# Kernel optimization log

Hardware: AMD Instinct MI355X
Metric: run time of the kernel (lower is better)

Reference implementation:

```python
import jax, jax.numpy as jnp
import numpy as np

DIM = 1024
HEADS = 16
DIM_HEAD = 64
INNER = HEADS * DIM_HEAD
EPS = 1e-5


def layernorm(x, g, b):
    mu = jnp.mean(x, axis=-1, keepdims=True)
    var = jnp.mean((x - mu) ** 2, axis=-1, keepdims=True)
    return (x - mu) * jax.lax.rsqrt(var + EPS) * g + b


def setup_inputs() -> dict:
    key = jax.random.key(0)
    ks = jax.random.split(key, 8)
    B, S = 2, 2048
    s_in = (2.0 / DIM) ** 0.5
    return {
        "x": jax.random.normal(ks[0], (B, S, DIM), jnp.float32),
        "w_qkv": jax.random.normal(ks[1], (DIM, 3 * INNER), jnp.float32) * s_in,
        "w_out": jax.random.normal(ks[2], (INNER, DIM), jnp.float32) * s_in,
        "b_out": jnp.zeros((DIM,), jnp.float32),
        "g1": jnp.ones((DIM,), jnp.float32),
        "beta1": jnp.zeros((DIM,), jnp.float32),
        "g2": jnp.ones((DIM,), jnp.float32),
        "beta2": jnp.zeros((DIM,), jnp.float32),
        "w_ff1": jax.random.normal(ks[3], (DIM, 4 * DIM), jnp.float32) * s_in,
        "b_ff1": jnp.zeros((4 * DIM,), jnp.float32),
        "w_ff2": jax.random.normal(ks[4], (4 * DIM, DIM), jnp.float32) * (2.0 / (4 * DIM)) ** 0.5,
        "b_ff2": jnp.zeros((DIM,), jnp.float32),
    }


def reference(x, w_qkv, w_out, b_out, g1, beta1, g2, beta2, w_ff1, b_ff1, w_ff2, b_ff2):
    B, S, D = x.shape
    scale = DIM_HEAD ** -0.5
    # --- attention block (pre-norm) ---
    h = layernorm(x, g1, beta1)
    qkv = h @ w_qkv  # [B,S,3*INNER]
    q, k, v = jnp.split(qkv, 3, axis=-1)
    def heads(t):
        return t.reshape(B, S, HEADS, DIM_HEAD).transpose(0, 2, 1, 3)  # [B,H,S,dh]
    q, k, v = heads(q), heads(k), heads(v)
    attn = jnp.einsum("bhsd,bhtd->bhst", q, k) * scale
    attn = jax.nn.softmax(attn, axis=-1)
    out = jnp.einsum("bhst,bhtd->bhsd", attn, v)
    out = out.transpose(0, 2, 1, 3).reshape(B, S, INNER)
    x = x + out @ w_out + b_out
    # --- FFN block (pre-norm) ---
    h = layernorm(x, g2, beta2)
    h = jax.nn.gelu(h @ w_ff1 + b_ff1, approximate=False)
    x = x + h @ w_ff2 + b_ff2
    return x
```

## Files before the change

### kernel.cpp

```cpp
#include <hip/hip_runtime.h>
#include <math.h>

typedef unsigned short u16;
typedef __attribute__((ext_vector_type(4))) float f32x4;
typedef __attribute__((ext_vector_type(16))) float f32x16;
typedef __attribute__((ext_vector_type(4))) unsigned short u16x4;
typedef __attribute__((ext_vector_type(8))) __bf16 bf16x8;

static constexpr int SS   = 2048;
static constexpr int DD   = 1024;
static constexpr int HH   = 16;
static constexpr int DH   = 64;
static constexpr int NTOK = 4096;
static constexpr int NQKV = 3072;

#define DEV static __device__ __forceinline__
#define GLD_AS1(p) ((__attribute__((address_space(1))) void*)(void*)(p))
#define GLD_AS3(p) ((__attribute__((address_space(3))) void*)(p))

#define WAIT_BAR(N) asm volatile("s_waitcnt vmcnt(" #N ")\n\ts_barrier" ::: "memory")
#define BAR()       asm volatile("s_barrier" ::: "memory")

DEV u16 f2bf(float f) {
    union { float f; unsigned int i; } v; v.f = f;
    unsigned int r = v.i + 0x7fffu + ((v.i >> 16) & 1u);
    return (u16)(r >> 16);
}
DEV float bdec(u16 u) {
    union { unsigned int i; float f; } v; v.i = ((unsigned int)u) << 16; return v.f;
}

DEV f32x4 MFMA(bf16x8 a, bf16x8 b, f32x4 c) {
    return __builtin_amdgcn_mfma_f32_16x16x32_bf16(a, b, c, 0, 0, 0);
}
DEV f32x16 MFMA32(bf16x8 a, bf16x8 b, f32x16 c) {
    return __builtin_amdgcn_mfma_f32_32x32x16_bf16(a, b, c, 0, 0, 0);
}
DEV f32x16 zero16() {
    f32x16 z;
    #pragma unroll
    for (int i = 0; i < 16; i++) z[i] = 0.f;
    return z;
}

__global__ __launch_bounds__(256)
void k_transpose(const float* __restrict__ in, u16* __restrict__ out, int R, int C) {
    __shared__ float tile[32][33];
    int c0 = blockIdx.x * 32, r0 = blockIdx.y * 32;
    int tx = threadIdx.x, ty = threadIdx.y;
    #pragma unroll
    for (int i = 0; i < 32; i += 8)
        tile[ty + i][tx] = in[(size_t)(r0 + ty + i) * C + c0 + tx];
    __syncthreads();
    #pragma unroll
    for (int i = 0; i < 32; i += 8)
        out[(size_t)(c0 + ty + i) * R + r0 + tx] = f2bf(tile[tx][ty + i]);
}

__global__ __launch_bounds__(256)
void k_transpose_v(const u16* __restrict__ qkv, u16* __restrict__ vT) {
    __shared__ u16 tile[32][33];
    int bid = blockIdx.x;
    int st = bid & 63;
    int dt = (bid >> 6) & 1;
    int bh = bid >> 7;
    int b = bh >> 4, h = bh & 15;
    int s0 = st * 32, d0 = dt * 32;
    int tx = threadIdx.x & 31, ty = threadIdx.x >> 5;
    const u16* src = qkv + ((size_t)(b * SS + s0)) * NQKV + 2048 + h * DH + d0;
    #pragma unroll
    for (int i = 0; i < 32; i += 8)
        tile[ty + i][tx] = src[(size_t)(ty + i) * NQKV + tx];
    __syncthreads();
    u16* dst = vT + ((size_t)bh * DH + d0) * SS + s0;
    #pragma unroll
    for (int i = 0; i < 32; i += 8)
        dst[(size_t)(ty + i) * SS + tx] = tile[tx][ty + i];
}

__global__ __launch_bounds__(256)
void k_layernorm(const float* __restrict__ x, const float* __restrict__ g,
                 const float* __restrict__ b, u16* __restrict__ out) {
    int row = blockIdx.x, t = threadIdx.x;
    const float4* xp = reinterpret_cast<const float4*>(x + (size_t)row * DD);
    float4 v = xp[t];
    float s = v.x + v.y + v.z + v.w;
    float q = v.x * v.x + v.y * v.y + v.z * v.z + v.w * v.w;
    #pragma unroll
    for (int m = 1; m < 64; m <<= 1) { s += __shfl_xor(s, m); q += __shfl_xor(q, m); }
    __shared__ float ps[4], pq[4];
    int w = t >> 6, l = t & 63;
    if (l == 0) { ps[w] = s; pq[w] = q; }
    __syncthreads();
    s = ps[0] + ps[1] + ps[2] + ps[3];
    q = pq[0] + pq[1] + pq[2] + pq[3];
    float mu = s * (1.0f / DD);
    float var = q * (1.0f / DD) - mu * mu;
    float rstd = rsqrtf(var + 1e-5f);
    float4 gv = reinterpret_cast<const float4*>(g)[t];
    float4 bv = reinterpret_cast<const float4*>(b)[t];
    u16x4 o;
    o.x = f2bf((v.x - mu) * rstd * gv.x + bv.x);
    o.y = f2bf((v.y - mu) * rstd * gv.y + bv.y);
    o.z = f2bf((v.z - mu) * rstd * gv.z + bv.z);
    o.w = f2bf((v.w - mu) * rstd * gv.w + bv.w);
    reinterpret_cast<u16x4*>(out + (size_t)row * DD)[t] = o;
}

__global__ __launch_bounds__(256)
void k_redln(const float* __restrict__ x, const u16* __restrict__ P0,
             const u16* __restrict__ P1, const float* __restrict__ bias,
             const float* __restrict__ g, const float* __restrict__ be,
             float* __restrict__ X1, u16* __restrict__ LNout) {
    int row = blockIdx.x, t = threadIdx.x;
    size_t i = (size_t)row * 256 + t;
    float4 xv = reinterpret_cast<const float4*>(x)[i];
    u16x4 a = reinterpret_cast<const u16x4*>(P0)[i];
    u16x4 bb = reinterpret_cast<const u16x4*>(P1)[i];
    float4 bv = reinterpret_cast<const float4*>(bias)[t];
    float4 v;
    v.x = xv.x + bdec(a.x) + bdec(bb.x) + bv.x;
    v.y = xv.y + bdec(a.y) + bdec(bb.y) + bv.y;
    v.z = xv.z + bdec(a.z) + bdec(bb.z) + bv.z;
    v.w = xv.w + bdec(a.w) + bdec(bb.w) + bv.w;
    reinterpret_cast<float4*>(X1)[i] = v;
    float s = v.x + v.y + v.z + v.w;
    float q = v.x * v.x + v.y * v.y + v.z * v.z + v.w * v.w;
    #pragma unroll
    for (int m = 1; m < 64; m <<= 1) { s += __shfl_xor(s, m); q += __shfl_xor(q, m); }
    __shared__ float ps[4], pq[4];
    int w = t >> 6, l = t & 63;
    if (l == 0) { ps[w] = s; pq[w] = q; }
    __syncthreads();
    s = ps[0] + ps[1] + ps[2] + ps[3];
    q = pq[0] + pq[1] + pq[2] + pq[3];
    float mu = s * (1.0f / DD);
    float var = q * (1.0f / DD) - mu * mu;
    float rstd = rsqrtf(var + 1e-5f);
    float4 gv = reinterpret_cast<const float4*>(g)[t];
    float4 ev = reinterpret_cast<const float4*>(be)[t];
    u16x4 o;
    o.x = f2bf((v.x - mu) * rstd * gv.x + ev.x);
    o.y = f2bf((v.y - mu) * rstd * gv.y + ev.y);
    o.z = f2bf((v.z - mu) * rstd * gv.z + ev.z);
    o.w = f2bf((v.w - mu) * rstd * gv.w + ev.w);
    reinterpret_cast<u16x4*>(LNout + (size_t)row * DD)[t] = o;
}

__global__ __launch_bounds__(256)
void k_gemm_qkv(const u16* __restrict__ A, const u16* __restrict__ BT,
                u16* __restrict__ Cb, int M, int N, int K) {
    __shared__ __align__(128) char lds[2][32768];
    const int t = threadIdx.x;
    const int w = t >> 6, l = t & 63;
    const int lg = l >> 4, lr = l & 15;
    const int GX = gridDim.x;
    const int T = GX * gridDim.y;
    const int H = blockIdx.x + blockIdx.y * GX;
    const int L = (H & 7) * (T >> 3) + (H >> 3);
    const int m0 = (L / GX) * 128, n0 = (L % GX) * 128;
    const int wr = w >> 1, wc = w & 1;

    const int csw = ((l & 7) ^ (l >> 3)) << 3;
    const int chunk0 = w * 4;
    const int srow = (l >> 3);

    f32x4 acc[4][4];
    #pragma unroll
    for (int i = 0; i < 4; i++)
        #pragma unroll
        for (int j = 0; j < 4; j++)
            acc[i][j] = (f32x4){0.f, 0.f, 0.f, 0.f};

    #pragma unroll
    for (int i = 0; i < 4; i++) {
        const int chunk = chunk0 + i;
        const int r = chunk * 8 + srow;
        __builtin_amdgcn_global_load_lds(GLD_AS1(A  + (size_t)(m0 + r) * K + csw),
                                         GLD_AS3(lds[0] + chunk * 1024), 16, 0, 0);
        __builtin_amdgcn_global_load_lds(GLD_AS1(BT + (size_t)(n0 + r) * K + csw),
                                         GLD_AS3(lds[0] + 16384 + chunk * 1024), 16, 0, 0);
    }

    int buf = 0;
    for (int kt = 0; kt < K; kt += 64) {
        if (kt + 64 < K) {
            #pragma unroll
            for (int i = 0; i < 4; i++) {
                const int chunk = chunk0 + i;
                const int r = chunk * 8 + srow;
                __builtin_amdgcn_global_load_lds(GLD_AS1(A  + (size_t)(m0 + r) * K + kt + 64 + csw),
                                                 GLD_AS3(lds[buf ^ 1] + chunk * 1024), 16, 0, 0);
                __builtin_amdgcn_global_load_lds(GLD_AS1(BT + (size_t)(n0 + r) * K + kt + 64 + csw),
                                                 GLD_AS3(lds[buf ^ 1] + 16384 + chunk * 1024), 16, 0, 0);
            }
            WAIT_BAR(8);
        } else {
            WAIT_BAR(0);
        }
        const char* Al = lds[buf];
        const char* Bl = lds[buf] + 16384;
        #pragma unroll
        for (int s = 0; s < 2; s++) {
            const int swz = (s * 64 + lg * 16) ^ ((lr & 7) << 4);
            bf16x8 af[4], bfr[4];
            #pragma unroll
            for (int mi = 0; mi < 4; mi++)
                af[mi] = *reinterpret_cast<const bf16x8*>(Al + (wr * 64 + mi * 16 + lr) * 128 + swz);
            #pragma unroll
            for (int ni = 0; ni < 4; ni++)
                bfr[ni] = *reinterpret_cast<const bf16x8*>(Bl + (wc * 64 + ni * 16 + lr) * 128 + swz);
            #pragma unroll
            for (int mi = 0; mi < 4; mi++)
                #pragma unroll
                for (int ni = 0; ni < 4; ni++)
                    acc[mi][ni] = MFMA(af[mi], bfr[ni], acc[mi][ni]);
        }
        BAR();
        buf ^= 1;
    }

    #pragma unroll
    for (int mi = 0; mi < 4; mi++) {
        #pragma unroll
        for (int ni = 0; ni < 4; ni++) {
            int nn = n0 + wc * 64 + ni * 16 + lr;
            #pragma unroll
            for (int r = 0; r < 4; r++) {
                int mm = m0 + wr * 64 + mi * 16 + lg * 4 + r;
                float v = acc[mi][ni][r];
                float sv = (nn < 1024) ? v * 0.18033688011112042f : v;
                Cb[(size_t)mm * NQKV + nn] = f2bf(sv);
            }
        }
    }
}

__global__ __launch_bounds__(512, 2)
void k_gemm_ff1(const u16* __restrict__ A, const u16* __restrict__ BT,
                u16* __restrict__ Cb, const float* __restrict__ bias,
                int M, int N, int K) {
    __shared__ __align__(128) char lds[2][65536];
    const int t = threadIdx.x;
    const int w = t >> 6, l = t & 63;
    const int lg = l >> 4, lr = l & 15;
    const int GX = gridDim.x;
    const int T = GX * gridDim.y;
    const int H = blockIdx.x + blockIdx.y * GX;
    const int L = (H & 7) * (T >> 3) + (H >> 3);
    const int m0 = (L / GX) * 256, n0 = (L % GX) * 256;
    const int wr = w >> 2, wc = w & 3;

    const int csw = ((l & 7) ^ (l >> 3)) << 3;
    const int srow8 = l >> 3;
    const int swzc = (lr & 7) << 4;

    f32x4 acc[8][4];
    #pragma unroll
    for (int i = 0; i < 8; i++)
        #pragma unroll
        for (int j = 0; j < 4; j++)
            acc[i][j] = (f32x4){0.f, 0.f, 0.f, 0.f};

    auto STAGEH = [&](int bf, int which, int half, int kt) {
        const u16* sb = which ? BT : A;
        const int rb = which ? n0 : m0;
        char* dst = lds[bf] + which * 32768 + half * 16384 + w * 1024;
        #pragma unroll
        for (int j = 0; j < 2; j++) {
            const int r = half * 128 + (j * 8 + w) * 8 + srow8;
            __builtin_amdgcn_global_load_lds(GLD_AS1(sb + (size_t)(rb + r) * K + kt + csw),
                                             GLD_AS3(dst + j * 8192), 16, 0, 0);
        }
    };

    STAGEH(0, 0, 0, 0); STAGEH(0, 0, 1, 0); STAGEH(0, 1, 0, 0); STAGEH(0, 1, 1, 0);

    const int nt = K >> 6;
    int buf = 0;
    for (int tt = 0; tt < nt; ++tt) {
        const int nb = buf ^ 1;
        const bool pre = (tt + 1 < nt);
        const char* Abase = lds[buf];
        const char* Bbase = lds[buf] + 32768;

        bf16x8 Bf[4][2];
        #pragma unroll
        for (int p = 0; p < 4; p++) {
            if (pre) STAGEH(nb, p >> 1, p & 1, (tt + 1) * 64);
            if (p == 0) {
                if (pre) { WAIT_BAR(2); } else { WAIT_BAR(0); }
                #pragma unroll
                for (int ni = 0; ni < 4; ni++)
                    #pragma unroll
                    for (int ks = 0; ks < 2; ks++)
                        Bf[ni][ks] = *reinterpret_cast<const bf16x8*>(
                            Bbase + (wc >> 1) * 16384 + ((wc & 1) * 64 + ni * 16 + lr) * 128
                                  + ((ks * 64 + lg * 16) ^ swzc));
            }
            bf16x8 Af[2][2];
            #pragma unroll
            for (int mi2 = 0; mi2 < 2; mi2++)
                #pragma unroll
                for (int ks = 0; ks < 2; ks++)
                    Af[mi2][ks] = *reinterpret_cast<const bf16x8*>(
                        Abase + wr * 16384 + ((p * 2 + mi2) * 16 + lr) * 128
                              + ((ks * 64 + lg * 16) ^ swzc));
            __builtin_amdgcn_s_setprio(1);
            #pragma unroll
            for (int mi2 = 0; mi2 < 2; mi2++)
                #pragma unroll
                for (int ni = 0; ni < 4; ni++)
                    #pragma unroll
                    for (int ks = 0; ks < 2; ks++)
                        acc[p * 2 + mi2][ni] = MFMA(Af[mi2][ks], Bf[ni][ks], acc[p * 2 + mi2][ni]);
            __builtin_amdgcn_s_setprio(0);
            BAR();
        }
        buf = nb;
    }

    #pragma unroll
    for (int mi = 0; mi < 8; mi++) {
        #pragma unroll
        for (int ni = 0; ni < 4; ni++) {
            int nn = n0 + wc * 64 + ni * 16 + lr;
            #pragma unroll
            for (int r = 0; r < 4; r++) {
                int mm = m0 + wr * 128 + mi * 16 + lg * 4 + r;
                float u = acc[mi][ni][r] + bias[nn];
                float u3 = u * u * u;
                float gl = u / (1.0f + exp2f(-2.3022077f * u - 0.10294276f * u3));
                Cb[(size_t)mm * N + nn] = f2bf(gl);
            }
        }
    }
}

__global__ __launch_bounds__(256)
void k_gemm_sk(const u16* __restrict__ A, const u16* __restrict__ BT,
               u16* __restrict__ P0, u16* __restrict__ P1, int M, int N, int K) {
    __shared__ __align__(128) char lds[2][32768];
    const int t = threadIdx.x;
    const int w = t >> 6, l = t & 63;
    const int lg = l >> 4, lr = l & 15;
    const int GX = gridDim.x, GY = gridDim.y;
    const int T = GX * GY * gridDim.z;
    const int H = blockIdx.x + blockIdx.y * GX + blockIdx.z * GX * GY;
    const int L = (H & 7) * (T >> 3) + (H >> 3);
    const int n0 = (L % GX) * 128;
    const int m0 = ((L / GX) % GY) * 128;
    const int zz = L / (GX * GY);
    const int wr = w >> 1, wc = w & 1;

    const int kh = K >> 1;
    const int kbeg = zz * kh;
    const int kend = kbeg + kh;

    const int csw = ((l & 7) ^ (l >> 3)) << 3;
    const int chunk0 = w * 4;
    const int srow = (l >> 3);

    f32x4 acc[4][4];
    #pragma unroll
    for (int i = 0; i < 4; i++)
        #pragma unroll
        for (int j = 0; j < 4; j++)
            acc[i][j] = (f32x4){0.f, 0.f, 0.f, 0.f};

    #pragma unroll
    for (int i = 0; i < 4; i++) {
        const int chunk = chunk0 + i;
        const int r = chunk * 8 + srow;
        __builtin_amdgcn_global_load_lds(GLD_AS1(A  + (size_t)(m0 + r) * K + kbeg + csw),
                                         GLD_AS3(lds[0] + chunk * 1024), 16, 0, 0);
        __builtin_amdgcn_global_load_lds(GLD_AS1(BT + (size_t)(n0 + r) * K + kbeg + csw),
                                         GLD_AS3(lds[0] + 16384 + chunk * 1024), 16, 0, 0);
    }

    int buf = 0;
    for (int kt = kbeg; kt < kend; kt += 64) {
        if (kt + 64 < kend) {
            #pragma unroll
            for (int i = 0; i < 4; i++) {
                const int chunk = chunk0 + i;
                const int r = chunk * 8 + srow;
                __builtin_amdgcn_global_load_lds(GLD_AS1(A  + (size_t)(m0 + r) * K + kt + 64 + csw),
                                                 GLD_AS3(lds[buf ^ 1] + chunk * 1024), 16, 0, 0);
                __builtin_amdgcn_global_load_lds(GLD_AS1(BT + (size_t)(n0 + r) * K + kt + 64 + csw),
                                                 GLD_AS3(lds[buf ^ 1] + 16384 + chunk * 1024), 16, 0, 0);
            }
            WAIT_BAR(8);
        } else {
            WAIT_BAR(0);
        }
        const char* Al = lds[buf];
        const char* Bl = lds[buf] + 16384;
        #pragma unroll
        for (int s = 0; s < 2; s++) {
            const int swz = (s * 64 + lg * 16) ^ ((lr & 7) << 4);
            bf16x8 af[4], bfr[4];
            #pragma unroll
            for (int mi = 0; mi < 4; mi++)
                af[mi] = *reinterpret_cast<const bf16x8*>(Al + (wr * 64 + mi * 16 + lr) * 128 + swz);
            #pragma unroll
            for (int ni = 0; ni < 4; ni++)
                bfr[ni] = *reinterpret_cast<const bf16x8*>(Bl + (wc * 64 + ni * 16 + lr) * 128 + swz);
            #pragma unroll
            for (int mi = 0; mi < 4; mi++)
                #pragma unroll
                for (int ni = 0; ni < 4; ni++)
                    acc[mi][ni] = MFMA(af[mi], bfr[ni], acc[mi][ni]);
        }
        BAR();
        buf ^= 1;
    }

    u16* dst = zz ? P1 : P0;
    #pragma unroll
    for (int mi = 0; mi < 4; mi++) {
        #pragma unroll
        for (int ni = 0; ni < 4; ni++) {
            int nn = n0 + wc * 64 + ni * 16 + lr;
            #pragma unroll
            for (int r = 0; r < 4; r++) {
                int mm = m0 + wr * 64 + mi * 16 + lg * 4 + r;
                dst[(size_t)mm * N + nn] = f2bf(acc[mi][ni][r]);
            }
        }
    }
}

__global__ __launch_bounds__(256)
void k_ffreduce(const float* __restrict__ RES, const u16* __restrict__ P0,
                const u16* __restrict__ P1, const float* __restrict__ bias,
                float* __restrict__ OUT) {
    int i = blockIdx.x * 256 + threadIdx.x;
    float4 xv = reinterpret_cast<const float4*>(RES)[i];
    u16x4 a = reinterpret_cast<const u16x4*>(P0)[i];
    u16x4 b = reinterpret_cast<const u16x4*>(P1)[i];
    float4 bv = reinterpret_cast<const float4*>(bias)[i & (DD / 4 - 1)];
    float4 o;
    o.x = xv.x + bdec(a.x) + bdec(b.x) + bv.x;
    o.y = xv.y + bdec(a.y) + bdec(b.y) + bv.y;
    o.z = xv.z + bdec(a.z) + bdec(b.z) + bv.z;
    o.w = xv.w + bdec(a.w) + bdec(b.w) + bv.w;
    reinterpret_cast<float4*>(OUT)[i] = o;
}

__global__ __launch_bounds__(256)
void k_attn(const u16* __restrict__ qkv, const u16* __restrict__ vT,
            u16* __restrict__ out) {
    const int w = threadIdx.x >> 6, l = threadIdx.x & 63;
    const int q = l & 31, hi = l >> 5;
    const int task = (blockIdx.x & 7) * 64 + (blockIdx.x >> 3);
    const int bh = task >> 4;
    const int qg = task & 15;
    const int b = bh >> 4, h = bh & 15;
    const size_t rowbase = (size_t)b * SS;
    const int q0 = (qg * 4 + w) * 32;

    __shared__ __align__(128) u16 Kl[3][64 * 64];
    __shared__ __align__(128) u16 Vl[2][64 * 64];

    const u16* kbase = qkv + rowbase * NQKV + 1024 + h * DH;
    const u16* vbase = vT + (size_t)bh * DH * SS;

    const int srow8 = l >> 3;
    const int sslot = (l & 7) ^ srow8;
    const int kr0 = w * 8 + srow8;
    const u16* kg0 = kbase + (size_t)kr0 * NQKV + sslot * 8;
    const u16* kg1 = kbase + (size_t)(kr0 + 32) * NQKV + sslot * 8;
    const u16* vg0 = vbase + (size_t)kr0 * SS + sslot * 8;
    const u16* vg1 = vbase + (size_t)(kr0 + 32) * SS + sslot * 8;
    const int chA = (w * 8) * 64, chB = (w * 8 + 32) * 64;

    const u16* qrow = qkv + (rowbase + q0 + q) * NQKV + h * DH + hi * 8;
    bf16x8 qf[4];
    #pragma unroll
    for (int ks = 0; ks < 4; ks++)
        qf[ks] = *reinterpret_cast<const bf16x8*>(qrow + ks * 16);
    asm volatile("s_waitcnt vmcnt(0)" ::: "memory");

    bf16x8 onesf;
    #pragma unroll
    for (int i = 0; i < 8; i++) onesf[i] = (__bf16)1.0f;

    f32x16 o0 = zero16(), o1 = zero16();
    f32x16 lacc = zero16();
    const int qsw = (q & 7) << 3;

    __builtin_amdgcn_global_load_lds(GLD_AS1(kg0), GLD_AS3((u16*)Kl[0] + chA), 16, 0, 0);
    __builtin_amdgcn_global_load_lds(GLD_AS1(kg1), GLD_AS3((u16*)Kl[0] + chB), 16, 0, 0);
    __builtin_amdgcn_global_load_lds(GLD_AS1(kg0 + (size_t)64 * NQKV), GLD_AS3((u16*)Kl[1] + chA), 16, 0, 0);
    __builtin_amdgcn_global_load_lds(GLD_AS1(kg1 + (size_t)64 * NQKV), GLD_AS3((u16*)Kl[1] + chB), 16, 0, 0);
    __builtin_amdgcn_global_load_lds(GLD_AS1(vg0), GLD_AS3((u16*)Vl[0] + chA), 16, 0, 0);
    __builtin_amdgcn_global_load_lds(GLD_AS1(vg1), GLD_AS3((u16*)Vl[0] + chB), 16, 0, 0);
    WAIT_BAR(4);

    f32x16 scA0 = zero16(), scA1 = zero16();
    {
        const u16* Kb = Kl[0];
        #pragma unroll
        for (int ks = 0; ks < 4; ks++) {
            const int off = (ks * 16 + hi * 8) ^ qsw;
            bf16x8 kf0 = *reinterpret_cast<const bf16x8*>(Kb + q * 64 + off);
            bf16x8 kf1 = *reinterpret_cast<const bf16x8*>(Kb + (q + 32) * 64 + off);
            scA0 = MFMA32(kf0, qf[ks], scA0);
            scA1 = MFMA32(kf1, qf[ks], scA1);
        }
    }

    int kRead = 1, vRead = 0;
    for (int i = 0; i < 32; ++i) {
        const int kStage = (kRead == 2) ? 0 : kRead + 1;
        if (i + 2 < 32) {
            const size_t koff = (size_t)(i + 2) * 64 * NQKV;
            __builtin_amdgcn_global_load_lds(GLD_AS1(kg0 + koff), GLD_AS3((u16*)Kl[kStage] + chA), 16, 0, 0);
            __builtin_amdgcn_global_load_lds(GLD_AS1(kg1 + koff), GLD_AS3((u16*)Kl[kStage] + chB), 16, 0, 0);
            WAIT_BAR(2);
        } else {
            WAIT_BAR(0);
        }
        if (i + 1 < 32) {
            const int voff = (i + 1) * 64;
            __builtin_amdgcn_global_load_lds(GLD_AS1(vg0 + voff), GLD_AS3((u16*)Vl[vRead ^ 1] + chA), 16, 0, 0);
            __builtin_amdgcn_global_load_lds(GLD_AS1(vg1 + voff), GLD_AS3((u16*)Vl[vRead ^ 1] + chB), 16, 0, 0);
        }

        f32x16 p0, p1;
        #pragma unroll
        for (int j = 0; j < 16; j++) p0[j] = exp2f(scA0[j]);
        #pragma unroll
        for (int j = 0; j < 16; j++) p1[j] = exp2f(scA1[j]);

        f32x16 stB0 = zero16(), stB1 = zero16();
        if (i + 1 < 32) {
            const u16* Kb = Kl[kRead];
            #pragma unroll
            for (int ks = 0; ks < 4; ks++) {
                const int off = (ks * 16 + hi * 8) ^ qsw;
                bf16x8 kf0 = *reinterpret_cast<const bf16x8*>(Kb + q * 64 + off);
                bf16x8 kf1 = *reinterpret_cast<const bf16x8*>(Kb + (q + 32) * 64 + off);
                stB0 = MFMA32(kf0, qf[ks], stB0);
                stB1 = MFMA32(kf1, qf[ks], stB1);
            }
        }

        union W { unsigned int u; __bf16 h[2]; };
        W pw[16];
        #pragma unroll
        for (int m = 0; m < 8; m++) {
            pw[m].h[0] = (__bf16)p0[2 * m];
            pw[m].h[1] = (__bf16)p0[2 * m + 1];
            pw[8 + m].h[0] = (__bf16)p1[2 * m];
            pw[8 + m].h[1] = (__bf16)p1[2 * m + 1];
        }

        bf16x8 pf[4];
        #pragma unroll
        for (int kk = 0; kk < 4; kk++) {
            const int base = (kk >> 1) * 8 + (kk & 1) * 4;
            unsigned int a0 = pw[base + 0].u, a1 = pw[base + 1].u;
            unsigned int b0 = pw[base + 2].u, b1 = pw[base + 3].u;
            unsigned int own0 = hi ? b0 : a0, own1 = hi ? b1 : a1;
            unsigned int snd0 = hi ? a0 : b0, snd1 = hi ? a1 : b1;
            unsigned int r0 = __shfl_xor(snd0, 32), r1 = __shfl_xor(snd1, 32);
            union F { unsigned int u[4]; bf16x8 v; } f;
            f.u[0] = hi ? r0 : own0;
            f.u[1] = hi ? r1 : own1;
            f.u[2] = hi ? own0 : r0;
            f.u[3] = hi ? own1 : r1;
            pf[kk] = f.v;
        }

        const u16* Vb = Vl[vRead];
        #pragma unroll
        for (int kk = 0; kk < 4; kk++) {
            const int off = (kk * 16 + hi * 8) ^ qsw;
            bf16x8 v0 = *reinterpret_cast<const bf16x8*>(Vb + q * 64 + off);
            bf16x8 v1 = *reinterpret_cast<const bf16x8*>(Vb + (q + 32) * 64 + off);
            lacc = MFMA32(onesf, pf[kk], lacc);
            o0 = MFMA32(v0, pf[kk], o0);
            o1 = MFMA32(v1, pf[kk], o1);
        }

        scA0 = stB0;
        scA1 = stB1;
        kRead = kStage;
        vRead ^= 1;
    }

    float invl = 1.0f / lacc[0];
    u16* orow = out + (rowbase + q0 + q) * DD + h * DH + hi * 4;
    #pragma unroll
    for (int a = 0; a < 4; a++) {
        u16x4 s0v, s1v;
        #pragma unroll
        for (int i = 0; i < 4; i++) {
            s0v[i] = f2bf(o0[4 * a + i] * invl);
            s1v[i] = f2bf(o1[4 * a + i] * invl);
        }
        *reinterpret_cast<u16x4*>(orow + 8 * a)      = s0v;
        *reinterpret_cast<u16x4*>(orow + 32 + 8 * a) = s1v;
    }
}

extern "C" void kernel_launch(void* const* d_in, const int* in_sizes, int n_in,
                              void* d_out, int out_size, void* d_ws, size_t ws_size,
                              hipStream_t stream) {
    (void)in_sizes; (void)n_in; (void)out_size; (void)ws_size;
    const float* x     = (const float*)d_in[0];
    const float* w_qkv = (const float*)d_in[1];
    const float* w_out = (const float*)d_in[2];
    const float* b_out = (const float*)d_in[3];
    const float* g1    = (const float*)d_in[4];
    const float* be1   = (const float*)d_in[5];
    const float* g2    = (const float*)d_in[6];
    const float* be2   = (const float*)d_in[7];
    const float* w_ff1 = (const float*)d_in[8];
    const float* b_ff1 = (const float*)d_in[9];
    const float* w_ff2 = (const float*)d_in[10];
    const float* b_ff2 = (const float*)d_in[11];

    char* ws = (char*)d_ws;
    u16*   W  = (u16*)(ws);
    u16*   Hb = (u16*)(ws + 8388608);
    u16*   QF = (u16*)(ws + 16777216);
    u16*   VT = (u16*)(ws + 50331648);
    u16*   AO = (u16*)(ws + 58720256);
    float* X1 = (float*)(ws + 67108864);
    float* OUT = (float*)d_out;

    k_layernorm<<<NTOK, 256, 0, stream>>>(x, g1, be1, Hb);
    k_transpose<<<dim3(3072 / 32, 1024 / 32), dim3(32, 8), 0, stream>>>(w_qkv, W, 1024, 3072);
    k_gemm_qkv<<<dim3(3072 / 128, 4096 / 128), 256, 0, stream>>>(
        Hb, W, QF, NTOK, NQKV, 1024);
    k_transpose_v<<<4096, 256, 0, stream>>>(QF, VT);
    k_attn<<<512, 256, 0, stream>>>(QF, VT, AO);
    k_transpose<<<dim3(1024 / 32, 1024 / 32), dim3(32, 8), 0, stream>>>(w_out, W, 1024, 1024);
    k_gemm_sk<<<dim3(1024 / 128, 4096 / 128, 2), 256, 0, stream>>>(
        AO, W, Hb, VT, NTOK, 1024, 1024);
    k_redln<<<NTOK, 256, 0, stream>>>(x, Hb, VT, b_out, g2, be2, X1, AO);
    k_transpose<<<dim3(4096 / 32, 1024 / 32), dim3(32, 8), 0, stream>>>(w_ff1, W, 1024, 4096);
    k_gemm_ff1<<<dim3(4096 / 256, 4096 / 256), 512, 0, stream>>>(
        AO, W, QF, b_ff1, NTOK, 4096, 1024);
    k_transpose<<<dim3(1024 / 32, 4096 / 32), dim3(32, 8), 0, stream>>>(w_ff2, W, 4096, 1024);
    k_gemm_sk<<<dim3(1024 / 128, 4096 / 128, 2), 256, 0, stream>>>(
        QF, W, VT, Hb, NTOK, 1024, 4096);
    k_ffreduce<<<NTOK * DD / 4 / 256, 256, 0, stream>>>(X1, VT, Hb, b_ff2, OUT);
}
```

Before: 249.9 us.

## Defer PV matmul by one iteration with four-stage V buffer in attention

Software-pipelines the attention loop so the P·V MFMA for tile i-1 runs while the exp of tile i and the QK^T for tile i+1 are in flight. The P fragments are carried across iterations, and V gets a 4-deep LDS ring so a single wait-plus-barrier per iteration can cover both the K and V loads. The goal is to overlap transcendental and MFMA work and to cut the number of barriers. In exchange it uses more LDS and registers, which may lower occupancy, and it adds a peeled epilogue after the loop.

```diff
diff --git a/kernel.cpp b/kernel.cpp
--- a/kernel.cpp
+++ b/kernel.cpp
@@ -461,7 +461,7 @@
     const int q0 = (qg * 4 + w) * 32;
 
     __shared__ __align__(128) u16 Kl[3][64 * 64];
-    __shared__ __align__(128) u16 Vl[2][64 * 64];
+    __shared__ __align__(128) u16 Vl[4][64 * 64];
 
     const u16* kbase = qkv + rowbase * NQKV + 1024 + h * DH;
     const u16* vbase = vT + (size_t)bh * DH * SS;
@@ -511,28 +511,42 @@
         }
     }
 
-    int kRead = 1, vRead = 0;
+    bf16x8 pfPrev[4];
+    int kRead = 1, kStage = 2;
     for (int i = 0; i < 32; ++i) {
-        const int kStage = (kRead == 2) ? 0 : kRead + 1;
         if (i + 2 < 32) {
             const size_t koff = (size_t)(i + 2) * 64 * NQKV;
             __builtin_amdgcn_global_load_lds(GLD_AS1(kg0 + koff), GLD_AS3((u16*)Kl[kStage] + chA), 16, 0, 0);
             __builtin_amdgcn_global_load_lds(GLD_AS1(kg1 + koff), GLD_AS3((u16*)Kl[kStage] + chB), 16, 0, 0);
-            WAIT_BAR(2);
-        } else {
-            WAIT_BAR(0);
         }
         if (i + 1 < 32) {
             const int voff = (i + 1) * 64;
-            __builtin_amdgcn_global_load_lds(GLD_AS1(vg0 + voff), GLD_AS3((u16*)Vl[vRead ^ 1] + chA), 16, 0, 0);
-            __builtin_amdgcn_global_load_lds(GLD_AS1(vg1 + voff), GLD_AS3((u16*)Vl[vRead ^ 1] + chB), 16, 0, 0);
-        }
+            u16* vdst = (u16*)Vl[(i + 1) & 3];
+            __builtin_amdgcn_global_load_lds(GLD_AS1(vg0 + voff), GLD_AS3(vdst + chA), 16, 0, 0);
+            __builtin_amdgcn_global_load_lds(GLD_AS1(vg1 + voff), GLD_AS3(vdst + chB), 16, 0, 0);
+        }
+        if (i < 30)      { WAIT_BAR(4); }
+        else if (i == 30){ WAIT_BAR(2); }
+        else             { WAIT_BAR(0); }
 
         f32x16 p0, p1;
         #pragma unroll
         for (int j = 0; j < 16; j++) p0[j] = exp2f(scA0[j]);
         #pragma unroll
         for (int j = 0; j < 16; j++) p1[j] = exp2f(scA1[j]);
+
+        if (i > 0) {
+            const u16* Vb = Vl[(i - 1) & 3];
+            #pragma unroll
+            for (int kk = 0; kk < 4; kk++) {
+                const int off = (kk * 16 + hi * 8) ^ qsw;
+                bf16x8 v0 = *reinterpret_cast<const bf16x8*>(Vb + q * 64 + off);
+                bf16x8 v1 = *reinterpret_cast<const bf16x8*>(Vb + (q + 32) * 64 + off);
+                lacc = MFMA32(onesf, pfPrev[kk], lacc);
+                o0 = MFMA32(v0, pfPrev[kk], o0);
+                o1 = MFMA32(v1, pfPrev[kk], o1);
+            }
+        }
 
         f32x16 stB0 = zero16(), stB1 = zero16();
         if (i + 1 < 32) {
@@ -556,8 +570,6 @@
             pw[8 + m].h[0] = (__bf16)p1[2 * m];
             pw[8 + m].h[1] = (__bf16)p1[2 * m + 1];
         }
-
-        bf16x8 pf[4];
         #pragma unroll
         for (int kk = 0; kk < 4; kk++) {
             const int base = (kk >> 1) * 8 + (kk & 1) * 4;
@@ -571,24 +583,26 @@
             f.u[1] = hi ? r1 : own1;
             f.u[2] = hi ? own0 : r0;
             f.u[3] = hi ? own1 : r1;
-            pf[kk] = f.v;
-        }
-
-        const u16* Vb = Vl[vRead];
+            pfPrev[kk] = f.v;
+        }
+
+        scA0 = stB0;
+        scA1 = stB1;
+        kRead = (kRead == 2) ? 0 : kRead + 1;
+        kStage = (kStage == 2) ? 0 : kStage + 1;
+    }
+
+    {
+        const u16* Vb = Vl[31 & 3];
         #pragma unroll
         for (int kk = 0; kk < 4; kk++) {
             const int off = (kk * 16 + hi * 8) ^ qsw;
             bf16x8 v0 = *reinterpret_cast<const bf16x8*>(Vb + q * 64 + off);
             bf16x8 v1 = *reinterpret_cast<const bf16x8*>(Vb + (q + 32) * 64 + off);
-            lacc = MFMA32(onesf, pf[kk], lacc);
-            o0 = MFMA32(v0, pf[kk], o0);
-            o1 = MFMA32(v1, pf[kk], o1);
-        }
-
-        scA0 = stB0;
-        scA1 = stB1;
-        kRead = kStage;
-        vRead ^= 1;
+            lacc = MFMA32(onesf, pfPrev[kk], lacc);
+            o0 = MFMA32(v0, pfPrev[kk], o0);
+            o1 = MFMA32(v1, pfPrev[kk], o1);
+        }
     }
 
     float invl = 1.0f / lacc[0];
```

After: 250.0 us. About the same (+0.0%).
